# Kernel optimization log

Hardware: AMD Instinct MI355X
Metric: run time of the kernel (lower is better)

The kernel has to match this reference:

```python
import jax, jax.numpy as jnp
import numpy as np

B, S, D, H = 2, 2048, 1024, 16
HD = D // H  # head_dim = 64


def setup_inputs() -> dict:
    key = jax.random.key(0)
    k1, k2, k3 = jax.random.split(key, 3)
    x = jax.random.normal(k1, (B, S, D), dtype=jnp.float32)
    W_qkv = jax.random.normal(k2, (D, 3 * D), dtype=jnp.float32) * (D ** -0.5)
    b_qkv = jnp.zeros((3 * D,), dtype=jnp.float32)
    W_proj = jax.random.normal(k3, (D, D), dtype=jnp.float32) * (D ** -0.5)
    b_proj = jnp.zeros((D,), dtype=jnp.float32)
    return {"x": x, "W_qkv": W_qkv, "b_qkv": b_qkv, "W_proj": W_proj, "b_proj": b_proj}


def reference(x, W_qkv, b_qkv, W_proj, b_proj):
    b, s, d = x.shape
    scale = HD ** -0.5
    qkv = x @ W_qkv + b_qkv                       # [B,S,3D]
    q, k, v = jnp.split(qkv, 3, axis=-1)
    # [B,S,D] -> [B,H,S,HD]
    def to_heads(t):
        return t.reshape(b, s, H, HD).transpose(0, 2, 1, 3)
    q, k, v = map(to_heads, (q, k, v))
    scores = jnp.einsum('bhqd,bhkd->bhqk', q, k) * scale  # [B,H,S,S]
    causal = jnp.triu(jnp.ones((s, s), dtype=bool), k=1)
    scores = jnp.where(causal[None, None], -jnp.inf, scores)
    attn = jax.nn.softmax(scores, axis=-1)
    out = jnp.einsum('bhqk,bhkd->bhqd', attn, v)  # [B,H,S,HD]
    out = out.transpose(0, 2, 1, 3).reshape(b, s, d)
    return out @ W_proj + b_proj
```

## Files before the change

kernel.cpp:

```cpp
#include <hip/hip_runtime.h>

using frag_t = __attribute__((ext_vector_type(8))) short;
using f32x4  = __attribute__((ext_vector_type(4))) float;

#define L2E 1.4426950408889634f

constexpr int B_  = 2, S_ = 2048, D_ = 1024, H_ = 16, HD_ = 64;
constexpr int M_  = B_ * S_;
constexpr float QSCALE = 0.125f * L2E;

__device__ __forceinline__ ushort f2bf(float f) {
  union { float f; unsigned u; } v; v.f = f;
  unsigned u = v.u;
  unsigned r = (u + 0x7FFFu + ((u >> 16) & 1u)) >> 16;
  return (ushort)r;
}
__device__ __forceinline__ ushort f2bf_fast(float f) {
  union { float f; unsigned u; } v; v.f = f;
  return (ushort)((v.u + 0x8000u) >> 16);
}

__device__ __forceinline__ void gld_lds16(const ushort* g, ushort* l) {
  __builtin_amdgcn_global_load_lds((const __attribute__((address_space(1))) void*)g,
                                   (__attribute__((address_space(3))) void*)l, 16, 0, 0);
}

__global__ void k_cvt_x(const float* __restrict__ in, ushort* __restrict__ out) {
  int idx = (blockIdx.x * 256 + threadIdx.x) * 4;
  float4 f = *(const float4*)(in + idx);
  ushort4 o;
  o.x = f2bf(f.x); o.y = f2bf(f.y); o.z = f2bf(f.z); o.w = f2bf(f.w);
  *(ushort4*)(out + idx) = o;
}

__global__ void k_tc(const float* __restrict__ in, ushort* __restrict__ out,
                     int N, int K) {
  __shared__ float tile[64][65];
  int n0 = blockIdx.x * 64, k0 = blockIdx.y * 64;
  int tx = threadIdx.x, ty = threadIdx.y;
  #pragma unroll
  for (int i = 0; i < 16; ++i)
    tile[ty + i * 4][tx] = in[(size_t)(k0 + ty + i * 4) * N + n0 + tx];
  __syncthreads();
  #pragma unroll
  for (int i = 0; i < 16; ++i)
    out[(size_t)(n0 + ty + i * 4) * K + k0 + tx] = f2bf(tile[tx][ty + i * 4]);
}

template <int EPI>
__global__ __launch_bounds__(256) void k_gemm(
    const ushort* __restrict__ A, const ushort* __restrict__ Bt,
    const float* __restrict__ bias,
    ushort* __restrict__ Qo, ushort* __restrict__ Ko, ushort* __restrict__ Vo,
    float* __restrict__ Co, int N, int K) {
  constexpr int BM = 128, BN = 128, BK = 64;
  constexpr int SMEM = (EPI == 0) ? 4 * 64 * 72 : (BM + BN) * BK;
  __shared__ ushort smem[SMEM];
  ushort* As = smem;
  ushort* Bs = smem + BM * BK;
  int tid  = threadIdx.x;
  int lane = tid & 63, wave = tid >> 6;
  int quad = lane >> 4, li = lane & 15;
  int wy = wave >> 1, wx = wave & 1;
  int m0 = blockIdx.y * BM, n0 = blockIdx.x * BN;
  int srow = lane >> 3;
  int scol = ((lane & 7) ^ srow) * 8;
  f32x4 acc[4][4] = {};
  for (int k0 = 0; k0 < K; k0 += BK) {
    #pragma unroll
    for (int i = 0; i < 4; ++i) {
      int rbase = i * 32 + wave * 8;
      int r = rbase + srow;
      gld_lds16(&A[(size_t)(m0 + r) * K + k0 + scol], &As[rbase * BK]);
      gld_lds16(&Bt[(size_t)(n0 + r) * K + k0 + scol], &Bs[rbase * BK]);
    }
    __syncthreads();
    #pragma unroll
    for (int ks = 0; ks < 2; ++ks) {
      frag_t af[4], bf[4];
      #pragma unroll
      for (int mi = 0; mi < 4; ++mi)
        af[mi] = *(const frag_t*)&As[(wy * 64 + mi * 16 + li) * BK + (((ks * 4 + quad) ^ (li & 7)) * 8)];
      #pragma unroll
      for (int ni = 0; ni < 4; ++ni)
        bf[ni] = *(const frag_t*)&Bs[(wx * 64 + ni * 16 + li) * BK + (((ks * 4 + quad) ^ (li & 7)) * 8)];
      #pragma unroll
      for (int mi = 0; mi < 4; ++mi)
        #pragma unroll
        for (int ni = 0; ni < 4; ++ni)
          acc[mi][ni] = __builtin_amdgcn_mfma_f32_16x16x32_bf16(af[mi], bf[ni], acc[mi][ni], 0, 0, 0);
    }
    __syncthreads();
  }
  if (EPI == 1) {
    #pragma unroll
    for (int mi = 0; mi < 4; ++mi)
      #pragma unroll
      for (int ni = 0; ni < 4; ++ni) {
        int gcol = n0 + wx * 64 + ni * 16 + li;
        float bv = bias[gcol];
        #pragma unroll
        for (int r = 0; r < 4; ++r) {
          int grow = m0 + wy * 64 + mi * 16 + quad * 4 + r;
          Co[(size_t)grow * N + gcol] = acc[mi][ni][r] + bv;
        }
      }
  } else {
    int which = (n0 + wx * 64) >> 10;
    if (which < 2) {
      #pragma unroll
      for (int mi = 0; mi < 4; ++mi)
        #pragma unroll
        for (int ni = 0; ni < 4; ++ni) {
          int gcol = n0 + wx * 64 + ni * 16 + li;
          float bv = bias[gcol];
          #pragma unroll
          for (int r = 0; r < 4; ++r) {
            int grow = m0 + wy * 64 + mi * 16 + quad * 4 + r;
            float v = acc[mi][ni][r] + bv;
            int d = gcol & 1023, h = d >> 6, hd = d & 63;
            int b = grow >> 11, s = grow & 2047;
            size_t bh = (size_t)b * H_ + h;
            if (which == 0) Qo[(bh * S_ + s) * HD_ + hd] = f2bf(v * QSCALE);
            else            Ko[(bh * S_ + s) * HD_ + hd] = f2bf(v);
          }
        }
    } else {
      ushort* vlds = smem + wave * (64 * 72);
      #pragma unroll
      for (int ni = 0; ni < 4; ++ni) {
        float bv = bias[n0 + wx * 64 + ni * 16 + li];
        #pragma unroll
        for (int mi = 0; mi < 4; ++mi)
          #pragma unroll
          for (int r = 0; r < 4; ++r)
            vlds[(ni * 16 + li) * 72 + mi * 16 + quad * 4 + r] = f2bf(acc[mi][ni][r] + bv);
      }
      int hgrp = ((n0 & 1023) + wx * 64) >> 6;
      int b = m0 >> 11;
      int s0 = (m0 & 2047) + wy * 64;
      size_t vbase = (size_t)(b * H_ + hgrp) * HD_ * S_;
      #pragma unroll
      for (int i = 0; i < 8; ++i) {
        int row = i * 8 + (lane >> 3);
        int col = (lane & 7) * 8;
        *(uint4*)&Vo[vbase + (size_t)row * S_ + s0 + col] = *(const uint4*)&vlds[row * 72 + col];
      }
    }
  }
}

__global__ __launch_bounds__(256) void k_attn(
    const ushort* __restrict__ Q, const ushort* __restrict__ K,
    const ushort* __restrict__ Vt, ushort* __restrict__ O) {
  __shared__ ushort Kbuf[2][64 * 64];
  __shared__ ushort Vbuf[2][64 * 64];
  __shared__ ushort Plds[4][16][72];
  int lane = threadIdx.x & 63, wave = threadIdx.x >> 6;
  int quad = lane >> 4, li = lane & 15;
  int bh = blockIdx.x;
  int qb = 31 - (int)blockIdx.y;
  int b = bh >> 4, h = bh & 15;
  int q0 = qb * 64 + wave * 16;
  const ushort* Qb = Q  + (size_t)bh * S_ * HD_;
  const ushort* Kb = K  + (size_t)bh * S_ * HD_;
  const ushort* Vb = Vt + (size_t)bh * HD_ * S_;

  frag_t qf[2];
  #pragma unroll
  for (int ks = 0; ks < 2; ++ks)
    qf[ks] = *(const frag_t*)&Qb[(size_t)(q0 + li) * HD_ + ks * 32 + quad * 8];

  f32x4 o[4] = {};
  float l_r[4] = {0.f, 0.f, 0.f, 0.f};

  auto stage = [&](int kb, int bi) {
    #pragma unroll
    for (int i = 0; i < 2; ++i) {
      int rt  = wave * 16 + i * 8 + (lane >> 3);
      int c16 = (lane & 7) ^ (lane >> 3);
      gld_lds16(&Kb[(size_t)(kb * 64 + rt) * HD_ + c16 * 8], &Kbuf[bi][(wave * 16 + i * 8) * 64]);
      gld_lds16(&Vb[(size_t)rt * S_ + kb * 64 + c16 * 8],    &Vbuf[bi][(wave * 16 + i * 8) * 64]);
    }
  };

  auto comp = [&](int kb, bool diag, int bi) {
    f32x4 sc[4];
    #pragma unroll
    for (int t = 0; t < 4; ++t) {
      f32x4 a = {};
      #pragma unroll
      for (int ks = 0; ks < 2; ++ks) {
        frag_t kf = *(const frag_t*)&Kbuf[bi][(t * 16 + li) * 64 + (((quad + ks * 4) ^ (li & 7)) * 8)];
        a = __builtin_amdgcn_mfma_f32_16x16x32_bf16(qf[ks], kf, a, 0, 0, 0);
      }
      sc[t] = a;
    }
    if (diag) {
      #pragma unroll
      for (int t = 0; t < 4; ++t) {
        int key = kb * 64 + t * 16 + li;
        #pragma unroll
        for (int r = 0; r < 4; ++r)
          if (key > q0 + quad * 4 + r) sc[t][r] = -1e30f;
      }
    }
    #pragma unroll
    for (int t = 0; t < 4; ++t)
      #pragma unroll
      for (int r = 0; r < 4; ++r) {
        float p = exp2f(sc[t][r]);
        l_r[r] += p;
        Plds[wave][quad * 4 + r][t * 16 + li] = f2bf_fast(p);
      }
    frag_t pf[2];
    #pragma unroll
    for (int ks = 0; ks < 2; ++ks)
      pf[ks] = *(const frag_t*)&Plds[wave][li][ks * 32 + quad * 8];
    #pragma unroll
    for (int t = 0; t < 4; ++t)
      #pragma unroll
      for (int ks = 0; ks < 2; ++ks) {
        frag_t vf = *(const frag_t*)&Vbuf[bi][(t * 16 + li) * 64 + (((quad + ks * 4) ^ (li & 7)) * 8)];
        o[t] = __builtin_amdgcn_mfma_f32_16x16x32_bf16(pf[ks], vf, o[t], 0, 0, 0);
      }
  };

  stage(0, 0);
  __syncthreads();
  for (int kb = 0; kb <= qb; ++kb) {
    if (kb < qb) stage(kb + 1, (kb + 1) & 1);
    comp(kb, kb == qb, kb & 1);
    __syncthreads();
  }

  #pragma unroll
  for (int r = 0; r < 4; ++r) {
    float t = l_r[r];
    #pragma unroll
    for (int off = 1; off < 16; off <<= 1) t += __shfl_xor(t, off);
    float inv = 1.f / t;
    int srow = q0 + quad * 4 + r;
    #pragma unroll
    for (int ht = 0; ht < 4; ++ht)
      O[((size_t)b * S_ + srow) * D_ + h * 64 + ht * 16 + li] = f2bf(o[ht][r] * inv);
  }
}

extern "C" void kernel_launch(void* const* d_in, const int* in_sizes, int n_in,
                              void* d_out, int out_size, void* d_ws, size_t ws_size,
                              hipStream_t stream) {
  (void)in_sizes; (void)n_in; (void)out_size; (void)ws_size;
  const float* x     = (const float*)d_in[0];
  const float* Wqkv  = (const float*)d_in[1];
  const float* bqkv  = (const float*)d_in[2];
  const float* Wproj = (const float*)d_in[3];
  const float* bproj = (const float*)d_in[4];
  float* out = (float*)d_out;

  char* ws = (char*)d_ws;
  ushort* Xbf = (ushort*)(ws);
  ushort* Wqt = (ushort*)(ws + (8u  << 20));
  ushort* Wpt = (ushort*)(ws + (14u << 20));
  ushort* Qbf = (ushort*)(ws + (16u << 20));
  ushort* Kbf = (ushort*)(ws + (24u << 20));
  ushort* Vtb = (ushort*)(ws + (32u << 20));
  ushort* Obf = Xbf;

  k_cvt_x<<<dim3(M_ * D_ / (256 * 4)), dim3(256), 0, stream>>>(x, Xbf);
  k_tc<<<dim3(48, 16), dim3(64, 4), 0, stream>>>(Wqkv, Wqt, 3 * D_, D_);
  k_tc<<<dim3(16, 16), dim3(64, 4), 0, stream>>>(Wproj, Wpt, D_, D_);
  k_gemm<0><<<dim3(24, 32), dim3(256), 0, stream>>>(Xbf, Wqt, bqkv, Qbf, Kbf, Vtb,
                                                    (float*)nullptr, 3 * D_, D_);
  k_attn<<<dim3(B_ * H_, 32), dim3(256), 0, stream>>>(Qbf, Kbf, Vtb, Obf);
  k_gemm<1><<<dim3(8, 32), dim3(256), 0, stream>>>(Obf, Wpt, bproj,
                                                   (ushort*)nullptr, (ushort*)nullptr, (ushort*)nullptr,
                                                   out, D_, D_);
}
```

Before: 194.2 us.

## Merge conversion/transpose prep kernels into one launch and swizzle attention P buffer

The three preprocessing launches (x conversion to bf16 and two weight transposes) are merged into a single kernel that dispatches on block index, removing two kernel launches and their gaps. Separately, the per-wave P staging buffer in attention drops its padded row layout in favour of an XOR-swizzled 64-wide layout, aimed at avoiding LDS bank conflicts on the scattered writes and the vector reads. The merged kernel puts blocks with different work and shared-memory needs into one grid, and the swizzle adds index arithmetic in the inner loop.

```diff
diff --git a/kernel.cpp b/kernel.cpp
--- a/kernel.cpp
+++ b/kernel.cpp
@@ -25,26 +25,35 @@
                                    (__attribute__((address_space(3))) void*)l, 16, 0, 0);
 }
 
-__global__ void k_cvt_x(const float* __restrict__ in, ushort* __restrict__ out) {
-  int idx = (blockIdx.x * 256 + threadIdx.x) * 4;
-  float4 f = *(const float4*)(in + idx);
-  ushort4 o;
-  o.x = f2bf(f.x); o.y = f2bf(f.y); o.z = f2bf(f.z); o.w = f2bf(f.w);
-  *(ushort4*)(out + idx) = o;
-}
-
-__global__ void k_tc(const float* __restrict__ in, ushort* __restrict__ out,
-                     int N, int K) {
-  __shared__ float tile[64][65];
-  int n0 = blockIdx.x * 64, k0 = blockIdx.y * 64;
-  int tx = threadIdx.x, ty = threadIdx.y;
-  #pragma unroll
-  for (int i = 0; i < 16; ++i)
-    tile[ty + i * 4][tx] = in[(size_t)(k0 + ty + i * 4) * N + n0 + tx];
-  __syncthreads();
-  #pragma unroll
-  for (int i = 0; i < 16; ++i)
-    out[(size_t)(n0 + ty + i * 4) * K + k0 + tx] = f2bf(tile[tx][ty + i * 4]);
+__global__ __launch_bounds__(256) void k_prep(
+    const float* __restrict__ x, const float* __restrict__ Wqkv,
+    const float* __restrict__ Wproj,
+    ushort* __restrict__ Xbf, ushort* __restrict__ Wqt, ushort* __restrict__ Wpt) {
+  int blk = blockIdx.x, tid = threadIdx.x;
+  if (blk < 1024) {
+    size_t base = (size_t)blk * 4096 + tid * 4;
+    #pragma unroll
+    for (int i = 0; i < 4; ++i) {
+      float4 f = *(const float4*)(x + base + i * 1024);
+      ushort4 o;
+      o.x = f2bf(f.x); o.y = f2bf(f.y); o.z = f2bf(f.z); o.w = f2bf(f.w);
+      *(ushort4*)(Xbf + base + i * 1024) = o;
+    }
+  } else {
+    __shared__ float tile[64][65];
+    const float* in; ushort* out; int N, K, bx, by;
+    if (blk < 1024 + 768) { int b2 = blk - 1024; in = Wqkv;  out = Wqt; N = 3072; K = 1024; bx = b2 % 48; by = b2 / 48; }
+    else                  { int b2 = blk - 1792; in = Wproj; out = Wpt; N = 1024; K = 1024; bx = b2 % 16; by = b2 / 16; }
+    int n0 = bx * 64, k0 = by * 64;
+    int tx = tid & 63, ty = tid >> 6;
+    #pragma unroll
+    for (int i = 0; i < 16; ++i)
+      tile[ty + i * 4][tx] = in[(size_t)(k0 + ty + i * 4) * N + n0 + tx];
+    __syncthreads();
+    #pragma unroll
+    for (int i = 0; i < 16; ++i)
+      out[(size_t)(n0 + ty + i * 4) * K + k0 + tx] = f2bf(tile[tx][ty + i * 4]);
+  }
 }
 
 template <int EPI>
@@ -155,7 +164,7 @@
     const ushort* __restrict__ Vt, ushort* __restrict__ O) {
   __shared__ ushort Kbuf[2][64 * 64];
   __shared__ ushort Vbuf[2][64 * 64];
-  __shared__ ushort Plds[4][16][72];
+  __shared__ ushort Plds[4 * 16 * 64];
   int lane = threadIdx.x & 63, wave = threadIdx.x >> 6;
   int quad = lane >> 4, li = lane & 15;
   int bh = blockIdx.x;
@@ -165,6 +174,7 @@
   const ushort* Qb = Q  + (size_t)bh * S_ * HD_;
   const ushort* Kb = K  + (size_t)bh * S_ * HD_;
   const ushort* Vb = Vt + (size_t)bh * HD_ * S_;
+  ushort* Pw = &Plds[wave * 1024];
 
   frag_t qf[2];
   #pragma unroll
@@ -211,12 +221,15 @@
       for (int r = 0; r < 4; ++r) {
         float p = exp2f(sc[t][r]);
         l_r[r] += p;
-        Plds[wave][quad * 4 + r][t * 16 + li] = f2bf_fast(p);
+        int row = quad * 4 + r;
+        int swr = ((row >> 2) << 1) | (row & 1);
+        Pw[row * 64 + (((t * 2 + (li >> 3)) ^ swr) * 8) + (li & 7)] = f2bf_fast(p);
       }
     frag_t pf[2];
+    int swl = ((li >> 2) << 1) | (li & 1);
     #pragma unroll
     for (int ks = 0; ks < 2; ++ks)
-      pf[ks] = *(const frag_t*)&Plds[wave][li][ks * 32 + quad * 8];
+      pf[ks] = *(const frag_t*)&Pw[li * 64 + (((ks * 4 + quad) ^ swl) * 8)];
     #pragma unroll
     for (int t = 0; t < 4; ++t)
       #pragma unroll
@@ -267,9 +280,7 @@
   ushort* Vtb = (ushort*)(ws + (32u << 20));
   ushort* Obf = Xbf;
 
-  k_cvt_x<<<dim3(M_ * D_ / (256 * 4)), dim3(256), 0, stream>>>(x, Xbf);
-  k_tc<<<dim3(48, 16), dim3(64, 4), 0, stream>>>(Wqkv, Wqt, 3 * D_, D_);
-  k_tc<<<dim3(16, 16), dim3(64, 4), 0, stream>>>(Wproj, Wpt, D_, D_);
+  k_prep<<<dim3(2048), dim3(256), 0, stream>>>(x, Wqkv, Wproj, Xbf, Wqt, Wpt);
   k_gemm<0><<<dim3(24, 32), dim3(256), 0, stream>>>(Xbf, Wqt, bqkv, Qbf, Kbf, Vtb,
                                                     (float*)nullptr, 3 * D_, D_);
   k_attn<<<dim3(B_ * H_, 32), dim3(256), 0, stream>>>(Qbf, Kbf, Vtb, Obf);
```

Result: faster. 190.0 us (-2.2%).
